# Performance work log

Measured on AMD Instinct MI355X. Metric: run time of the kernel, lower is better.

Reference implementation:

```python
import jax, jax.numpy as jnp
import numpy as np

H, L, NH, DH, FF, V, MAXP = 768, 2, 12, 64, 3072, 50265, 512
B, S = 64, 512


def _ln(x, g, b, eps=1e-5):
    mu = jnp.mean(x, axis=-1, keepdims=True)
    var = jnp.mean(jnp.square(x - mu), axis=-1, keepdims=True)
    return (x - mu) * jax.lax.rsqrt(var + eps) * g + b


def setup_inputs() -> dict:
    key = jax.random.key(0)
    ks = jax.random.split(key, 16)
    sd = 0.02
    inp = {
        "source_ids": jax.random.randint(ks[0], (B, S), 0, V),
        "position_idx": jax.random.randint(ks[1], (B, S), 0, MAXP),
        "attn_mask": jax.random.randint(ks[2], (B, S, S), 0, 2).astype(bool),
        "word_emb": sd * jax.random.normal(ks[3], (V, H), jnp.float32),
        "pos_emb": sd * jax.random.normal(ks[4], (MAXP, H), jnp.float32),
        "ln_g": jnp.ones((H,), jnp.float32),
        "ln_b": jnp.zeros((H,), jnp.float32),
        "Wqkv": sd * jax.random.normal(ks[5], (L, H, 3 * H), jnp.float32),
        "bqkv": jnp.zeros((L, 3 * H), jnp.float32),
        "Wo": sd * jax.random.normal(ks[6], (L, H, H), jnp.float32),
        "bo": jnp.zeros((L, H), jnp.float32),
        "ln1_g": jnp.ones((L, H), jnp.float32),
        "ln1_b": jnp.zeros((L, H), jnp.float32),
        "W1": sd * jax.random.normal(ks[7], (L, H, FF), jnp.float32),
        "b1": jnp.zeros((L, FF), jnp.float32),
        "W2": sd * jax.random.normal(ks[8], (L, FF, H), jnp.float32),
        "b2": jnp.zeros((L, H), jnp.float32),
        "ln2_g": jnp.ones((L, H), jnp.float32),
        "ln2_b": jnp.zeros((L, H), jnp.float32),
        "dense_W": sd * jax.random.normal(ks[9], (H, H), jnp.float32),
        "dense_b": jnp.zeros((H,), jnp.float32),
        "out_W": sd * jax.random.normal(ks[10], (H, 1), jnp.float32),
        "out_b": jnp.zeros((1,), jnp.float32),
    }
    return inp


def reference(source_ids, position_idx, attn_mask, word_emb, pos_emb, ln_g, ln_b,
              Wqkv, bqkv, Wo, bo, ln1_g, ln1_b, W1, b1, W2, b2, ln2_g, ln2_b,
              dense_W, dense_b, out_W, out_b):
    nodes_mask = position_idx == 0          # [B,S] bool
    token_mask = position_idx >= 2          # [B,S] bool
    emb = word_emb[source_ids]              # [B,S,H]

    # node -> token masked mean aggregation (the custom-kernel hotspot)
    m = (nodes_mask[:, :, None] & token_mask[:, None, :] & attn_mask).astype(emb.dtype)  # [B,S,S]
    w = m / (jnp.sum(m, axis=-1, keepdims=True) + 1e-10)
    avg = jnp.einsum('bnt,btd->bnd', w, emb)
    nm = nodes_mask[:, :, None].astype(emb.dtype)
    emb = emb * (1.0 - nm) + avg * nm

    # RoBERTa-style embeddings: inputs_embeds + position embeddings, layernorm
    h = _ln(emb + pos_emb[position_idx], ln_g, ln_b)

    # additive attention bias from 3D mask
    bias = jnp.where(attn_mask, 0.0, -1e4).astype(h.dtype)[:, None, :, :]  # [B,1,S,S]
    scale = 1.0 / np.sqrt(DH)

    for l in range(L):
        qkv = h @ Wqkv[l] + bqkv[l]                     # [B,S,3H]
        q, k, v = jnp.split(qkv, 3, axis=-1)
        q = q.reshape(B, S, NH, DH)
        k = k.reshape(B, S, NH, DH)
        v = v.reshape(B, S, NH, DH)
        scores = jnp.einsum('bqhd,bkhd->bhqk', q, k) * scale + bias
        attn = jax.nn.softmax(scores, axis=-1)
        ctx = jnp.einsum('bhqk,bkhd->bqhd', attn, v).reshape(B, S, H)
        h = _ln(h + ctx @ Wo[l] + bo[l], ln1_g[l], ln1_b[l])
        ffn = jax.nn.gelu(h @ W1[l] + b1[l], approximate=False) @ W2[l] + b2[l]
        h = _ln(h + ffn, ln2_g[l], ln2_b[l])

    # classification head (dropout in eval = identity)
    x = h[:, 0, :]
    x = jnp.tanh(x @ dense_W + dense_b)
    logits = x @ out_W + out_b                          # [B,1]
    return logits
```

## Files before the change

### kernel.cpp

```cpp
#include <hip/hip_runtime.h>

typedef unsigned short u16;
typedef unsigned int   u32;
typedef __bf16 bf16x8 __attribute__((ext_vector_type(8)));
typedef float  f32x4  __attribute__((ext_vector_type(4)));

#define DEVI __device__ __forceinline__

DEVI u16 f2bf(float f){
  u32 u = __builtin_bit_cast(u32, f);
  u32 r = (u + 0x7fffu + ((u >> 16) & 1u)) >> 16;
  return (u16)r;
}
DEVI float bf2f(u16 u){
  u32 x = ((u32)u) << 16;
  return __builtin_bit_cast(float, x);
}

DEVI void gload16(const void* g, void* lds){
  __builtin_amdgcn_global_load_lds(
      (const __attribute__((address_space(1))) void*)g,
      (__attribute__((address_space(3))) void*)lds, 16, 0, 0);
}

DEVI f32x4 MFMA(bf16x8 a, bf16x8 b, f32x4 c){
  return __builtin_amdgcn_mfma_f32_16x16x32_bf16(a, b, c, 0, 0, 0);
}

#define BAR() do { asm volatile("s_barrier" ::: "memory"); \
                   __builtin_amdgcn_sched_barrier(0); } while(0)

__global__ void k_maskprobe(const unsigned char* __restrict__ m, int* __restrict__ flag){
  __shared__ int s;
  if (threadIdx.x == 0) s = 0;
  __syncthreads();
  int acc = 0;
  for (int i = threadIdx.x; i < 65536; i += 256)
    if ((i & 3) != 0 && m[i] != 0) acc++;
  atomicAdd(&s, acc);
  __syncthreads();
  if (threadIdx.x == 0) *flag = (s > 0) ? 1 : 0;
}

__global__ void k_maskbits(const void* __restrict__ mask, const int* __restrict__ flag,
                           u32* __restrict__ mb){
  int row  = blockIdx.x * 4 + (threadIdx.x >> 6);
  int lane = threadIdx.x & 63;
  bool bytes = (*flag != 0);
  for (int c0 = 0; c0 < 512; c0 += 64){
    int v;
    if (bytes) v = ((const unsigned char*)mask)[(size_t)row * 512 + c0 + lane];
    else       v = ((const int*)mask)[(size_t)row * 512 + c0 + lane];
    unsigned long long bits = __ballot(v != 0);
    if (lane == 0){
      mb[(size_t)row * 16 + (c0 >> 5)]     = (u32)(bits & 0xffffffffull);
      mb[(size_t)row * 16 + (c0 >> 5) + 1] = (u32)(bits >> 32);
    }
  }
}

__global__ void k_embed(const int* __restrict__ ids, const float* __restrict__ wemb,
                        float* __restrict__ h){
  int row = blockIdx.x;
  const float* s = wemb + (size_t)ids[row] * 768;
  float* d = h + (size_t)row * 768;
  int t = threadIdx.x;
  d[t] = s[t]; d[t + 256] = s[t + 256]; d[t + 512] = s[t + 512];
}

__global__ void k_nodeavg(const int* __restrict__ pos, const u32* __restrict__ mb,
                          float* __restrict__ h){
  int row = blockIdx.x;
  if (pos[row] != 0) return;
  int b = row >> 9;
  int c = blockIdx.y * 256 + threadIdx.x;
  const u32* mrow = mb + (size_t)row * 16;
  const int* pb = pos + ((size_t)b << 9);
  float a = 0.f, cnt = 0.f;
  #pragma unroll 4
  for (int t = 0; t < 512; t++){
    if (pb[t] >= 2 && ((mrow[t >> 5] >> (t & 31)) & 1)){
      a += h[(((size_t)b << 9) + t) * 768 + c];
      cnt += 1.f;
    }
  }
  h[(size_t)row * 768 + c] = a / (cnt + 1e-10f);
}

__global__ void k_ln0(const int* __restrict__ pos, const float* __restrict__ pemb,
                      const float* __restrict__ g, const float* __restrict__ be,
                      const float* __restrict__ h, u16* __restrict__ hb){
  __shared__ float s1[4], s2[4];
  int row = blockIdx.x, t = threadIdx.x;
  const float* hr = h + (size_t)row * 768;
  const float* pr = pemb + (size_t)pos[row] * 768;
  float x0 = hr[t] + pr[t], x1 = hr[t+256] + pr[t+256], x2 = hr[t+512] + pr[t+512];
  float s = x0 + x1 + x2, q = x0*x0 + x1*x1 + x2*x2;
  for (int o = 32; o; o >>= 1){ s += __shfl_down(s, o, 64); q += __shfl_down(q, o, 64); }
  int wv = t >> 6, ln = t & 63;
  if (!ln){ s1[wv] = s; s2[wv] = q; }
  __syncthreads();
  s = s1[0]+s1[1]+s1[2]+s1[3]; q = s2[0]+s2[1]+s2[2]+s2[3];
  float mu = s * (1.f/768.f);
  float rs = rsqrtf(q * (1.f/768.f) - mu*mu + 1e-5f);
  u16* hbr = hb + (size_t)row * 768;
  hbr[t]     = f2bf((x0-mu)*rs*g[t]     + be[t]);
  hbr[t+256] = f2bf((x1-mu)*rs*g[t+256] + be[t+256]);
  hbr[t+512] = f2bf((x2-mu)*rs*g[t+512] + be[t+512]);
}

__global__ void k_lnres(const float* __restrict__ C, const float* __restrict__ g,
                        const float* __restrict__ be, u16* __restrict__ hb){
  __shared__ float s1[4], s2[4];
  int row = blockIdx.x, t = threadIdx.x;
  u16* hr = hb + (size_t)row * 768;
  const float* cr = C + (size_t)row * 768;
  float x0 = bf2f(hr[t])     + cr[t];
  float x1 = bf2f(hr[t+256]) + cr[t+256];
  float x2 = bf2f(hr[t+512]) + cr[t+512];
  float s = x0 + x1 + x2, q = x0*x0 + x1*x1 + x2*x2;
  for (int o = 32; o; o >>= 1){ s += __shfl_down(s, o, 64); q += __shfl_down(q, o, 64); }
  int wv = t >> 6, ln = t & 63;
  if (!ln){ s1[wv] = s; s2[wv] = q; }
  __syncthreads();
  s = s1[0]+s1[1]+s1[2]+s1[3]; q = s2[0]+s2[1]+s2[2]+s2[3];
  float mu = s * (1.f/768.f);
  float rs = rsqrtf(q * (1.f/768.f) - mu*mu + 1e-5f);
  hr[t]     = f2bf((x0-mu)*rs*g[t]     + be[t]);
  hr[t+256] = f2bf((x1-mu)*rs*g[t+256] + be[t+256]);
  hr[t+512] = f2bf((x2-mu)*rs*g[t+512] + be[t+512]);
}

__global__ void k_transpose(const float* __restrict__ src, u16* __restrict__ dst,
                            int K, int N){
  __shared__ float tile[32][33];
  int k0 = blockIdx.x * 32, n0 = blockIdx.y * 32;
  int tx = threadIdx.x & 31, ty = threadIdx.x >> 5;
  #pragma unroll
  for (int i = 0; i < 32; i += 8)
    tile[ty + i][tx] = src[(size_t)(k0 + ty + i) * N + n0 + tx];
  __syncthreads();
  #pragma unroll
  for (int i = 0; i < 32; i += 8)
    dst[(size_t)(n0 + ty + i) * K + k0 + tx] = f2bf(tile[tx][ty + i]);
}


DEVI void stageA32(const u16* __restrict__ src, int K, u16* lds, int tid){
  int r = tid >> 2, c = tid & 3;
  int sc = c ^ ((r >> 1) & 3);
  gload16(src + (size_t)r*K + sc*8, lds + (size_t)tid*8);
}
DEVI void stageB32(const u16* __restrict__ src, int K, u16* lds, int tid){
  #pragma unroll
  for (int j = 0; j < 2; j++){
    int p = j*512 + tid;
    int r = p >> 2, c = p & 3;
    int sc = c ^ ((r >> 1) & 3);
    gload16(src + (size_t)r*K + sc*8, lds + (size_t)p*8);
  }
}

template<int EPI>
__global__ __launch_bounds__(512, 4)
void k_gemm3(const u16* __restrict__ A, const u16* __restrict__ BT,
             const float* __restrict__ bias, void* __restrict__ out,
             int M, int N, int K){
  __shared__ __align__(16) u16 sm[36864];
  const int tid = threadIdx.x;
  const int w = tid >> 6, lane = tid & 63;
  const int wm = w >> 2, wn = w & 3;
  const int cr = lane & 15, cg = lane >> 4;

  const int nbn = gridDim.x;
  const int nwg = nbn * gridDim.y;
  const int d   = blockIdx.y * nbn + blockIdx.x;
  const int xcd = d & 7, qq = nwg >> 3, rr = nwg & 7;
  const int logical = (xcd < rr ? xcd*(qq+1) : rr*(qq+1) + (xcd-rr)*qq) + (d >> 3);
  const int m0 = (logical / nbn) * 128;
  const int n0 = (logical % nbn) * 256;

  const int NT = K >> 5;
  const u16* Abase = A  + (size_t)m0 * K;
  const u16* Bbase = BT + (size_t)n0 * K;
  const int rowA = wm*64 + cr;
  const int rowB = wn*64 + cr;

  f32x4 acc[4][4] = {};
  bf16x8 afr[4], bfr[4];

  stageA32(Abase, K, sm, tid);
  stageB32(Bbase, K, sm + 12288, tid);
  if (NT > 1){
    stageA32(Abase + 32, K, sm + 4096, tid);
    stageB32(Bbase + 32, K, sm + 12288 + 8192, tid);
    asm volatile("s_waitcnt vmcnt(3)" ::: "memory");
  } else {
    asm volatile("s_waitcnt vmcnt(0)" ::: "memory");
  }
  __builtin_amdgcn_sched_barrier(0);
  BAR();

  int bcur = 0;
  for (int t = 0; t < NT; ++t){
    const int ab = bcur << 12;
    const int bb = 12288 + (bcur << 13);
    int bn2 = bcur + 2; if (bn2 >= 3) bn2 -= 3;

    #pragma unroll
    for (int n = 0; n < 4; n++){
      int r = rowB + n*16;
      bfr[n] = *(const bf16x8*)&sm[bb + r*32 + ((cg ^ ((r >> 1) & 3)) << 3)];
    }
    #pragma unroll
    for (int i = 0; i < 4; i++){
      int r = rowA + i*16;
      afr[i] = *(const bf16x8*)&sm[ab + r*32 + ((cg ^ ((r >> 1) & 3)) << 3)];
    }
    if (t + 2 < NT){
      stageA32(Abase + (size_t)(t+2)*32, K, sm + (bn2 << 12), tid);
      stageB32(Bbase + (size_t)(t+2)*32, K, sm + 12288 + (bn2 << 13), tid);
    }

    __builtin_amdgcn_s_setprio(1);
    #pragma unroll
    for (int i = 0; i < 4; i++)
      #pragma unroll
      for (int n = 0; n < 4; n++)
        acc[i][n] = MFMA(afr[i], bfr[n], acc[i][n]);
    __builtin_amdgcn_s_setprio(0);

    if (t + 2 < NT) { asm volatile("s_waitcnt vmcnt(3)" ::: "memory"); }
    else            { asm volatile("s_waitcnt vmcnt(0)" ::: "memory"); }
    __builtin_amdgcn_sched_barrier(0);
    BAR();
    bcur = bcur + 1; if (bcur >= 3) bcur = 0;
  }

  if (EPI == 1){
    #pragma unroll
    for (int n = 0; n < 4; n++){
      int col = n0 + wn*64 + n*16 + cr;
      float bv = bias[col];
      #pragma unroll
      for (int i = 0; i < 4; i++){
        #pragma unroll
        for (int j = 0; j < 4; j++){
          int row = m0 + wm*64 + i*16 + cg*4 + j;
          ((float*)out)[(size_t)row * N + col] = acc[i][n][j] + bv;
        }
      }
    }
  } else {
    const int LDC = 264;
    #pragma unroll
    for (int n = 0; n < 4; n++){
      int coll = wn*64 + n*16 + cr;
      float bv = bias[n0 + coll];
      #pragma unroll
      for (int i = 0; i < 4; i++){
        #pragma unroll
        for (int j = 0; j < 4; j++){
          int rowl = wm*64 + i*16 + cg*4 + j;
          float v = acc[i][n][j] + bv;
          if (EPI == 2) v = 0.5f * v * (1.f + erff(v * 0.70710678118654752f));
          sm[rowl*LDC + coll] = f2bf(v);
        }
      }
    }
    BAR();
    if (EPI == 3){
      #pragma unroll
      for (int it = 0; it < 8; it++){
        int idx = it*512 + tid;
        int c = idx & 7, hh2 = (idx >> 3) & 3, s = idx >> 5;
        uint4 v4 = *(const uint4*)&sm[s*LDC + hh2*64 + c*8];
        int col0 = n0 + hh2*64;
        int sec = (col0 >= 1536) ? 2 : (col0 >= 768 ? 1 : 0);
        int hd  = (col0 - sec*768) >> 6;
        int row = m0 + s;
        int b = row >> 9, sr = row & 511;
        *(uint4*)((u16*)out + (size_t)sec*25165824 +
                  (((size_t)(b*12 + hd)*512 + sr) << 6) + c*8) = v4;
      }
    } else {
      #pragma unroll
      for (int it = 0; it < 8; it++){
        int idx = it*512 + tid;
        int r = idx >> 5, c8 = idx & 31;
        uint4 v4 = *(const uint4*)&sm[r*LDC + c8*8];
        *(uint4*)((u16*)out + (size_t)(m0 + r)*N + n0 + c8*8) = v4;
      }
    }
  }
}

__global__ void k_vtrep(const u16* __restrict__ vbuf, u16* __restrict__ vt){
  __shared__ u16 tile[64][72];
  int bh = blockIdx.y;
  int t0 = blockIdx.x * 64;
  int tid = threadIdx.x;
  #pragma unroll
  for (int i = 0; i < 16; i++){
    int idx = tid + i * 256;
    int tt = idx >> 6, d = idx & 63;
    tile[tt][d] = vbuf[((size_t)bh * 512 + t0 + tt) * 64 + d];
  }
  __syncthreads();
  #pragma unroll
  for (int i = 0; i < 16; i++){
    int idx = tid + i * 256;
    int d = idx >> 6, tt = idx & 63;
    vt[((size_t)bh * 64 + d) * 512 + t0 + tt] = tile[tt][d];
  }
}

DEVI void stage64(const u16* __restrict__ src, int stride, u16* lds, int w, int lane){
  #pragma unroll
  for (int j = 0; j < 2; j++){
    int p  = j*256 + w*64 + lane;
    int r  = p >> 3;
    int c8 = (p & 7) ^ (r & 7);
    gload16(src + (size_t)r*stride + c8*8, lds + (size_t)p*8);
  }
}

__global__ __launch_bounds__(256, 4)
void k_attn3(const u16* __restrict__ qp, const u16* __restrict__ kp,
             const u16* __restrict__ vt, const u32* __restrict__ mb,
             u16* __restrict__ ctx){
  __shared__ __align__(16) u16 Ks[8192];
  __shared__ __align__(16) u16 Vs[8192];
  const int tid = threadIdx.x, wv = tid >> 6, lane = tid & 63;
  const int cr = lane & 15, cg = lane >> 4;
  const int cg4 = cg * 4;
  const int r7 = cr & 7;

  const int dd = blockIdx.x + (blockIdx.y << 3);
  const int logical = (dd & 7) * 768 + (dd >> 3);
  const int bh = logical >> 3;
  const int qblk = logical & 7;
  const int b = bh / 12, hh = bh % 12;
  const int qw = qblk * 64 + wv * 16;
  const int qrow = qw + cr;
  const size_t base = (size_t)bh * 512 * 64;
  const u16* vtb = vt + (size_t)bh * 64 * 512;

  const int slot0 = ((cg    ) ^ r7) << 3;
  const int slot1 = ((4 + cg) ^ r7) << 3;

  bf16x8 qB[2];
  #pragma unroll
  for (int ks = 0; ks < 2; ks++)
    qB[ks] = *(const bf16x8*)&qp[base + (size_t)qrow * 64 + ks*32 + cg*8];

  u32 mw[16];
  {
    const u32* mrow = mb + ((size_t)b * 512 + qrow) * 16;
    #pragma unroll
    for (int i = 0; i < 4; i++){
      uint4 v4 = *(const uint4*)&mrow[i*4];
      mw[i*4+0] = v4.x; mw[i*4+1] = v4.y; mw[i*4+2] = v4.z; mw[i*4+3] = v4.w;
    }
  }

  stage64(kp + base, 64, Ks, wv, lane);
  stage64(vtb,      512, Vs, wv, lane);
  asm volatile("s_waitcnt vmcnt(0)" ::: "memory");
  __builtin_amdgcn_sched_barrier(0);
  BAR();

  float m = -3e38f, vs = 0.f;
  f32x4 oacc[4] = {};

  for (int s = 0; s < 8; ++s){
    const int buf = (s & 1) << 12;
    const int nbf = ((s + 1) & 1) << 12;

    if (s + 1 < 8){
      stage64(kp + base + (size_t)(s+1)*4096, 64, Ks + nbf, wv, lane);
      stage64(vtb + (size_t)(s+1)*64,        512, Vs + nbf, wv, lane);
    }

    f32x4 pacc[4];
    #pragma unroll
    for (int tt = 0; tt < 4; tt++){
      bf16x8 a0 = *(const bf16x8*)&Ks[buf + (tt*16 + cr)*64 + slot0];
      bf16x8 a1 = *(const bf16x8*)&Ks[buf + (tt*16 + cr)*64 + slot1];
      f32x4 z = {0.f, 0.f, 0.f, 0.f};
      z = MFMA(a0, qB[0], z);
      z = MFMA(a1, qB[1], z);
      pacc[tt] = z;
    }

    const u32 w0 = mw[2*s], w1 = mw[2*s+1];
    f32x4 vmx = {-3e38f, -3e38f, -3e38f, -3e38f};
    #pragma unroll
    for (int tt = 0; tt < 4; tt++){
      u32 nib = (((tt < 2) ? w0 : w1) >> (16*(tt & 1) + cg4)) & 0xFu;
      #pragma unroll
      for (int j = 0; j < 4; j++){
        float v = pacc[tt][j] * 0.125f + (((nib >> j) & 1u) ? 0.f : -10000.f);
        pacc[tt][j] = v;
        vmx[j] = fmaxf(vmx[j], v);
      }
    }
    float tm = fmaxf(fmaxf(vmx[0], vmx[1]), fmaxf(vmx[2], vmx[3]));
    tm = fmaxf(tm, __shfl_xor(tm, 16, 64));
    tm = fmaxf(tm, __shfl_xor(tm, 32, 64));

    float mnew = fmaxf(m, tm);
    float alpha = __expf(m - mnew);
    m = mnew;
    #pragma unroll
    for (int db = 0; db < 4; db++) oacc[db] *= alpha;

    f32x4 vsum = {0.f, 0.f, 0.f, 0.f};
    #pragma unroll
    for (int tt = 0; tt < 4; tt++){
      #pragma unroll
      for (int j = 0; j < 4; j++){
        float e = __expf(pacc[tt][j] - m);
        pacc[tt][j] = e;
        vsum[j] += e;
      }
    }
    vs = vs * alpha + (vsum[0] + vsum[1] + vsum[2] + vsum[3]);

    bf16x8 pa[2];
    #pragma unroll
    for (int c = 0; c < 2; c++)
      #pragma unroll
      for (int e = 0; e < 4; e++){
        pa[c][e]   = (__bf16)pacc[2*c][e];
        pa[c][4+e] = (__bf16)pacc[2*c+1][e];
      }

    #pragma unroll
    for (int c = 0; c < 2; c++){
      const int ch0 = ((4*c     + (cg >> 1)) ^ r7);
      const int ch1 = ((4*c + 2 + (cg >> 1)) ^ r7);
      const int sub = (cg & 1) << 3;
      #pragma unroll
      for (int db = 0; db < 4; db++){
        const char* vrow = (const char*)&Vs[buf + (db*16 + cr)*64];
        bf16x8 vb;
        ((uint2*)&vb)[0] = *(const uint2*)(vrow + (ch0 << 4) + sub);
        ((uint2*)&vb)[1] = *(const uint2*)(vrow + (ch1 << 4) + sub);
        oacc[db] = MFMA(pa[c], vb, oacc[db]);
      }
    }

    if (s + 1 < 8) { asm volatile("s_waitcnt vmcnt(0)" ::: "memory"); }
    __builtin_amdgcn_sched_barrier(0);
    BAR();
  }

  vs += __shfl_xor(vs, 16, 64);
  vs += __shfl_xor(vs, 32, 64);
  #pragma unroll
  for (int j = 0; j < 4; j++){
    float ds = __shfl(vs, cg4 + j, 64);
    float inv = 1.0f / ds;
    #pragma unroll
    for (int db = 0; db < 4; db++)
      ctx[((size_t)b * 512 + qw + cg4 + j) * 768 + hh*64 + 16*db + cr] = f2bf(oacc[db][j] * inv);
  }
}

__global__ __launch_bounds__(256)
void k_dense(const u16* __restrict__ hb, const float* __restrict__ W,
             const float* __restrict__ bias, float* __restrict__ xt){
  __shared__ float xs[768];
  __shared__ float red[256];
  const int b = blockIdx.y, t = threadIdx.x;
  const u16* hr = hb + (size_t)b * 512 * 768;
  xs[t] = bf2f(hr[t]); xs[t+256] = bf2f(hr[t+256]); xs[t+512] = bf2f(hr[t+512]);
  __syncthreads();
  const int col = blockIdx.x * 64 + (t & 63);
  const int ks  = t >> 6;
  const float* Wp = W + (size_t)(ks * 192) * 768 + col;
  const float* xp = xs + ks * 192;
  float a = 0.f;
  #pragma unroll 8
  for (int k = 0; k < 192; k++) a += xp[k] * Wp[(size_t)k * 768];
  red[t] = a;
  __syncthreads();
  if (t < 64){
    float y = red[t] + red[t+64] + red[t+128] + red[t+192] + bias[col];
    xt[(size_t)b * 768 + col] = tanhf(y);
  }
}

__global__ void k_logits(const float* __restrict__ xt, const float* __restrict__ ow,
                         const float* __restrict__ ob, float* __restrict__ out){
  __shared__ float sb[4];
  int b = blockIdx.x, t = threadIdx.x;
  const float* x = xt + (size_t)b * 768;
  float s = x[t]*ow[t] + x[t+256]*ow[t+256] + x[t+512]*ow[t+512];
  for (int o = 32; o; o >>= 1) s += __shfl_down(s, o, 64);
  int wv = t >> 6, ln = t & 63;
  if (!ln) sb[wv] = s;
  __syncthreads();
  if (t == 0) out[b] = sb[0] + sb[1] + sb[2] + sb[3] + ob[0];
}

extern "C" void kernel_launch(void* const* d_in, const int* in_sizes, int n_in,
                              void* d_out, int out_size, void* d_ws, size_t ws_size,
                              hipStream_t stream){
  if (n_in < 23) return;
  if (ws_size < 534000000ull) return;

  const int*   ids  = (const int*)  d_in[0];
  const int*   pos  = (const int*)  d_in[1];
  const void*  amsk =               d_in[2];
  const float* wemb = (const float*)d_in[3];
  const float* pemb = (const float*)d_in[4];
  const float* lng  = (const float*)d_in[5];
  const float* lnb  = (const float*)d_in[6];
  const float* Wqkv = (const float*)d_in[7];
  const float* bqkv = (const float*)d_in[8];
  const float* Wo   = (const float*)d_in[9];
  const float* bo   = (const float*)d_in[10];
  const float* ln1g = (const float*)d_in[11];
  const float* ln1b = (const float*)d_in[12];
  const float* W1   = (const float*)d_in[13];
  const float* b1   = (const float*)d_in[14];
  const float* W2   = (const float*)d_in[15];
  const float* b2   = (const float*)d_in[16];
  const float* ln2g = (const float*)d_in[17];
  const float* ln2b = (const float*)d_in[18];
  const float* dW   = (const float*)d_in[19];
  const float* db   = (const float*)d_in[20];
  const float* oW   = (const float*)d_in[21];
  const float* ob   = (const float*)d_in[22];

  char* ws = (char*)d_ws;
  float* h    = (float*)(ws);
  u16*   hb   = (u16*)  (ws + 100663296);
  float* C    = (float*)(ws + 150994944);
  u16*   qkvp = (u16*)  (ws + 251658240);
  u16*   vt   = (u16*)  (ws + 402653184);
  u16*   act  = (u16*)  (ws + 251658240);
  u16*   ctx  = (u16*)  (ws + 452984832);
  u32*   mbit = (u32*)  (ws + 503316480);
  u16*   wt   = (u16*)  (ws + 505413632);
  float* xt   = (float*)(ws + 533725184);
  int*   flag = (int*)  (ws + 533921792);

  u16* qp   = qkvp;
  u16* kp   = qkvp + (size_t)25165824;
  u16* vbuf = qkvp + (size_t)50331648;

  u16* WqkvT = wt;
  u16* WoT   = WqkvT + (size_t)2*2304*768;
  u16* W1T   = WoT   + (size_t)2*768*768;
  u16* W2T   = W1T   + (size_t)2*3072*768;

  k_maskprobe<<<1, 256, 0, stream>>>((const unsigned char*)amsk, flag);
  k_maskbits<<<8192, 256, 0, stream>>>(amsk, flag, mbit);

  for (int l = 0; l < 2; l++){
    k_transpose<<<dim3(24, 72), 256, 0, stream>>>(Wqkv + (size_t)l*768*2304, WqkvT + (size_t)l*2304*768, 768, 2304);
    k_transpose<<<dim3(24, 24), 256, 0, stream>>>(Wo   + (size_t)l*768*768,  WoT   + (size_t)l*768*768,  768, 768);
    k_transpose<<<dim3(24, 96), 256, 0, stream>>>(W1   + (size_t)l*768*3072, W1T   + (size_t)l*3072*768, 768, 3072);
    k_transpose<<<dim3(96, 24), 256, 0, stream>>>(W2   + (size_t)l*3072*768, W2T   + (size_t)l*768*3072, 3072, 768);
  }

  k_embed<<<32768, 256, 0, stream>>>(ids, wemb, h);
  k_nodeavg<<<dim3(32768, 3), 256, 0, stream>>>(pos, mbit, h);
  k_ln0<<<32768, 256, 0, stream>>>(pos, pemb, lng, lnb, h, hb);

  for (int l = 0; l < 2; l++){
    k_gemm3<3><<<dim3(9, 256), 512, 0, stream>>>(hb, WqkvT + (size_t)l*2304*768, bqkv + l*2304, (void*)qkvp, 32768, 2304, 768);
    k_vtrep<<<dim3(8, 768), 256, 0, stream>>>(vbuf, vt);
    k_attn3<<<dim3(8, 768), 256, 0, stream>>>(qp, kp, vt, mbit, ctx);
    k_gemm3<1><<<dim3(3, 256), 512, 0, stream>>>(ctx, WoT + (size_t)l*768*768, bo + l*768, (void*)C, 32768, 768, 768);
    k_lnres<<<32768, 256, 0, stream>>>(C, ln1g + l*768, ln1b + l*768, hb);
    k_gemm3<2><<<dim3(12, 256), 512, 0, stream>>>(hb, W1T + (size_t)l*3072*768, b1 + l*3072, (void*)act, 32768, 3072, 768);
    k_gemm3<1><<<dim3(3, 256), 512, 0, stream>>>(act, W2T + (size_t)l*768*3072, b2 + l*768, (void*)C, 32768, 768, 3072);
    k_lnres<<<32768, 256, 0, stream>>>(C, ln2g + l*768, ln2b + l*768, hb);
  }

  k_dense<<<dim3(12, 64), 256, 0, stream>>>(hb, dW, db, xt);
  k_logits<<<64, 256, 0, stream>>>(xt, oW, ob, (float*)d_out);
}
```

Baseline: 1.888 ms.

## Fuse embedding, node averaging and layernorm; write transposed V from QKV GEMM

Combines the embedding gather, node-to-token masked averaging and the first layernorm into one kernel, so the fp32 h buffer is never written and re-read. Node rows now gather word embeddings straight from the table, multiplying each token row by a 0/1 weight, which reads all 512 token rows unconditionally. The QKV GEMM epilogue now writes V blocks directly in transposed [bh, d, s] layout through a padded LDS stride, which removes the separate k_vtrep pass and its round trip through global memory. The transposed epilogue uses scalar LDS gathers, which may slow that epilogue.

```diff
diff --git a/kernel.cpp b/kernel.cpp
--- a/kernel.cpp
+++ b/kernel.cpp
@@ -59,42 +59,35 @@
   }
 }
 
-__global__ void k_embed(const int* __restrict__ ids, const float* __restrict__ wemb,
-                        float* __restrict__ h){
-  int row = blockIdx.x;
-  const float* s = wemb + (size_t)ids[row] * 768;
-  float* d = h + (size_t)row * 768;
-  int t = threadIdx.x;
-  d[t] = s[t]; d[t + 256] = s[t + 256]; d[t + 512] = s[t + 512];
-}
-
-__global__ void k_nodeavg(const int* __restrict__ pos, const u32* __restrict__ mb,
-                          float* __restrict__ h){
-  int row = blockIdx.x;
-  if (pos[row] != 0) return;
-  int b = row >> 9;
-  int c = blockIdx.y * 256 + threadIdx.x;
-  const u32* mrow = mb + (size_t)row * 16;
-  const int* pb = pos + ((size_t)b << 9);
-  float a = 0.f, cnt = 0.f;
-  #pragma unroll 4
-  for (int t = 0; t < 512; t++){
-    if (pb[t] >= 2 && ((mrow[t >> 5] >> (t & 31)) & 1)){
-      a += h[(((size_t)b << 9) + t) * 768 + c];
-      cnt += 1.f;
-    }
-  }
-  h[(size_t)row * 768 + c] = a / (cnt + 1e-10f);
-}
-
-__global__ void k_ln0(const int* __restrict__ pos, const float* __restrict__ pemb,
-                      const float* __restrict__ g, const float* __restrict__ be,
-                      const float* __restrict__ h, u16* __restrict__ hb){
+__global__ void k_embln(const int* __restrict__ ids, const int* __restrict__ pos,
+                        const u32* __restrict__ mb, const float* __restrict__ wemb,
+                        const float* __restrict__ pemb, const float* __restrict__ g,
+                        const float* __restrict__ be, u16* __restrict__ hb){
   __shared__ float s1[4], s2[4];
   int row = blockIdx.x, t = threadIdx.x;
-  const float* hr = h + (size_t)row * 768;
-  const float* pr = pemb + (size_t)pos[row] * 768;
-  float x0 = hr[t] + pr[t], x1 = hr[t+256] + pr[t+256], x2 = hr[t+512] + pr[t+512];
+  int p = pos[row];
+  float x0, x1, x2;
+  if (p == 0){
+    int b = row >> 9;
+    const u32* mrow = mb + (size_t)row * 16;
+    const int* pb = pos + ((size_t)b << 9);
+    const int* ib = ids + ((size_t)b << 9);
+    float a0 = 0.f, a1 = 0.f, a2 = 0.f, cnt = 0.f;
+    #pragma unroll 8
+    for (int k = 0; k < 512; k++){
+      float w = (pb[k] >= 2 && ((mrow[k >> 5] >> (k & 31)) & 1)) ? 1.f : 0.f;
+      const float* src = wemb + (size_t)ib[k] * 768;
+      a0 += w * src[t]; a1 += w * src[t+256]; a2 += w * src[t+512];
+      cnt += w;
+    }
+    float inv = 1.f / (cnt + 1e-10f);
+    x0 = a0 * inv; x1 = a1 * inv; x2 = a2 * inv;
+  } else {
+    const float* src = wemb + (size_t)ids[row] * 768;
+    x0 = src[t]; x1 = src[t+256]; x2 = src[t+512];
+  }
+  const float* pr = pemb + (size_t)p * 768;
+  x0 += pr[t]; x1 += pr[t+256]; x2 += pr[t+512];
   float s = x0 + x1 + x2, q = x0*x0 + x1*x1 + x2*x2;
   for (int o = 32; o; o >>= 1){ s += __shfl_down(s, o, 64); q += __shfl_down(q, o, 64); }
   int wv = t >> 6, ln = t & 63;
@@ -165,7 +158,7 @@
 __global__ __launch_bounds__(512, 4)
 void k_gemm3(const u16* __restrict__ A, const u16* __restrict__ BT,
              const float* __restrict__ bias, void* __restrict__ out,
-             int M, int N, int K){
+             void* __restrict__ out2, int M, int N, int K){
   __shared__ __align__(16) u16 sm[36864];
   const int tid = threadIdx.x;
   const int w = tid >> 6, lane = tid & 63;
@@ -252,7 +245,8 @@
       }
     }
   } else {
-    const int LDC = 264;
+    const bool vblk = (EPI == 3) && (n0 >= 1536);
+    const int LDC = vblk ? 266 : 264;
     #pragma unroll
     for (int n = 0; n < 4; n++){
       int coll = wn*64 + n*16 + cr;
@@ -270,48 +264,45 @@
     }
     BAR();
     if (EPI == 3){
-      #pragma unroll
-      for (int it = 0; it < 8; it++){
-        int idx = it*512 + tid;
-        int c = idx & 7, hh2 = (idx >> 3) & 3, s = idx >> 5;
-        uint4 v4 = *(const uint4*)&sm[s*LDC + hh2*64 + c*8];
-        int col0 = n0 + hh2*64;
-        int sec = (col0 >= 1536) ? 2 : (col0 >= 768 ? 1 : 0);
-        int hd  = (col0 - sec*768) >> 6;
-        int row = m0 + s;
-        int b = row >> 9, sr = row & 511;
-        *(uint4*)((u16*)out + (size_t)sec*25165824 +
-                  (((size_t)(b*12 + hd)*512 + sr) << 6) + c*8) = v4;
+      int b = m0 >> 9, s0 = m0 & 511;
+      if (vblk){
+        int hd0 = (n0 - 1536) >> 6;
+        int dl = lane >> 2, sc4 = lane & 3;
+        #pragma unroll
+        for (int it = 0; it < 8; it++){
+          int gidx = it*8 + w;
+          int hh2 = gidx >> 4, dhi = (gidx >> 2) & 3, shi = gidx & 3;
+          int dd2 = dhi*16 + dl;
+          int schunk = shi*4 + sc4;
+          u16 tmp[8];
+          #pragma unroll
+          for (int k = 0; k < 8; k++)
+            tmp[k] = sm[(schunk*8 + k)*266 + hh2*64 + dd2];
+          *(uint4*)((u16*)out2 + (((size_t)(b*12 + hd0 + hh2)*64 + dd2) << 9)
+                    + s0 + schunk*8) = *(uint4*)tmp;
+        }
+      } else {
+        #pragma unroll
+        for (int it = 0; it < 8; it++){
+          int idx = it*512 + tid;
+          int c = idx & 7, hh2 = (idx >> 3) & 3, s = idx >> 5;
+          uint4 v4 = *(const uint4*)&sm[s*264 + hh2*64 + c*8];
+          int col0 = n0 + hh2*64;
+          int sec = (col0 >= 768) ? 1 : 0;
+          int hd  = (col0 - sec*768) >> 6;
+          *(uint4*)((u16*)out + (size_t)sec*25165824 +
+                    (((size_t)(b*12 + hd)*512 + (m0 & 511) + s) << 6) + c*8) = v4;
+        }
       }
     } else {
       #pragma unroll
       for (int it = 0; it < 8; it++){
         int idx = it*512 + tid;
         int r = idx >> 5, c8 = idx & 31;
-        uint4 v4 = *(const uint4*)&sm[r*LDC + c8*8];
+        uint4 v4 = *(const uint4*)&sm[r*264 + c8*8];
         *(uint4*)((u16*)out + (size_t)(m0 + r)*N + n0 + c8*8) = v4;
       }
     }
-  }
-}
-
-__global__ void k_vtrep(const u16* __restrict__ vbuf, u16* __restrict__ vt){
-  __shared__ u16 tile[64][72];
-  int bh = blockIdx.y;
-  int t0 = blockIdx.x * 64;
-  int tid = threadIdx.x;
-  #pragma unroll
-  for (int i = 0; i < 16; i++){
-    int idx = tid + i * 256;
-    int tt = idx >> 6, d = idx & 63;
-    tile[tt][d] = vbuf[((size_t)bh * 512 + t0 + tt) * 64 + d];
-  }
-  __syncthreads();
-  #pragma unroll
-  for (int i = 0; i < 16; i++){
-    int idx = tid + i * 256;
-    int d = idx >> 6, tt = idx & 63;
-    vt[((size_t)bh * 64 + d) * 512 + t0 + tt] = tile[tt][d];
   }
 }
 
@@ -536,7 +527,6 @@
   const float* ob   = (const float*)d_in[22];
 
   char* ws = (char*)d_ws;
-  float* h    = (float*)(ws);
   u16*   hb   = (u16*)  (ws + 100663296);
   float* C    = (float*)(ws + 150994944);
   u16*   qkvp = (u16*)  (ws + 251658240);
@@ -550,7 +540,6 @@
 
   u16* qp   = qkvp;
   u16* kp   = qkvp + (size_t)25165824;
-  u16* vbuf = qkvp + (size_t)50331648;
 
   u16* WqkvT = wt;
   u16* WoT   = WqkvT + (size_t)2*2304*768;
@@ -567,18 +556,15 @@
     k_transpose<<<dim3(96, 24), 256, 0, stream>>>(W2   + (size_t)l*3072*768, W2T   + (size_t)l*768*3072, 3072, 768);
   }
 
-  k_embed<<<32768, 256, 0, stream>>>(ids, wemb, h);
-  k_nodeavg<<<dim3(32768, 3), 256, 0, stream>>>(pos, mbit, h);
-  k_ln0<<<32768, 256, 0, stream>>>(pos, pemb, lng, lnb, h, hb);
+  k_embln<<<32768, 256, 0, stream>>>(ids, pos, mbit, wemb, pemb, lng, lnb, hb);
 
   for (int l = 0; l < 2; l++){
-    k_gemm3<3><<<dim3(9, 256), 512, 0, stream>>>(hb, WqkvT + (size_t)l*2304*768, bqkv + l*2304, (void*)qkvp, 32768, 2304, 768);
-    k_vtrep<<<dim3(8, 768), 256, 0, stream>>>(vbuf, vt);
+    k_gemm3<3><<<dim3(9, 256), 512, 0, stream>>>(hb, WqkvT + (size_t)l*2304*768, bqkv + l*2304, (void*)qkvp, (void*)vt, 32768, 2304, 768);
     k_attn3<<<dim3(8, 768), 256, 0, stream>>>(qp, kp, vt, mbit, ctx);
-    k_gemm3<1><<<dim3(3, 256), 512, 0, stream>>>(ctx, WoT + (size_t)l*768*768, bo + l*768, (void*)C, 32768, 768, 768);
+    k_gemm3<1><<<dim3(3, 256), 512, 0, stream>>>(ctx, WoT + (size_t)l*768*768, bo + l*768, (void*)C, nullptr, 32768, 768, 768);
     k_lnres<<<32768, 256, 0, stream>>>(C, ln1g + l*768, ln1b + l*768, hb);
-    k_gemm3<2><<<dim3(12, 256), 512, 0, stream>>>(hb, W1T + (size_t)l*3072*768, b1 + l*3072, (void*)act, 32768, 3072, 768);
-    k_gemm3<1><<<dim3(3, 256), 512, 0, stream>>>(act, W2T + (size_t)l*768*3072, b2 + l*768, (void*)C, 32768, 768, 3072);
+    k_gemm3<2><<<dim3(12, 256), 512, 0, stream>>>(hb, W1T + (size_t)l*3072*768, b1 + l*3072, (void*)act, nullptr, 32768, 3072, 768);
+    k_gemm3<1><<<dim3(3, 256), 512, 0, stream>>>(act, W2T + (size_t)l*768*3072, b2 + l*768, (void*)C, nullptr, 32768, 768, 3072);
     k_lnres<<<32768, 256, 0, stream>>>(C, ln2g + l*768, ln2b + l*768, hb);
   }
 
```

Result: faster. 1.757 ms (-7.0%).
